# Optimization experiments

Measured on AMD Instinct MI355X. Metric: run time of the kernel, lower is better.

The kernel has to match this reference:

```python
import jax, jax.numpy as jnp
import numpy as np
from jax import lax

B, T, D_MODEL = 4, 2048, 2048
EXPAND, D_CONV = 2, 4
D_INNER = D_MODEL * EXPAND


def setup_inputs() -> dict:
    key = jax.random.key(0)
    ks = jax.random.split(key, 5)
    x = jax.random.normal(ks[0], (B, T, D_MODEL), dtype=jnp.float32)
    w_in = jax.random.normal(ks[1], (2 * D_INNER, D_MODEL), dtype=jnp.float32) * (D_MODEL ** -0.5)
    w_out = jax.random.normal(ks[2], (D_MODEL, D_INNER), dtype=jnp.float32) * (D_INNER ** -0.5)
    conv_w = jax.random.normal(ks[3], (D_INNER, 1, D_CONV), dtype=jnp.float32) * (D_CONV ** -0.5)
    conv_b = jax.random.normal(ks[4], (D_INNER,), dtype=jnp.float32) * 0.02
    D = jnp.ones((D_INNER,), dtype=jnp.float32)
    return {"x": x, "w_in": w_in, "w_out": w_out, "conv_w": conv_w, "conv_b": conv_b, "D": D}


def _forward(x, w_in, w_out, conv_w, conv_b, D):
    # in_proj: [B,T,C] @ [C, 2*d_inner]
    x_proj = jnp.einsum('btc,dc->btd', x, w_in)
    xi, gate = jnp.split(x_proj, 2, axis=-1)  # each [B,T,d_inner]
    # depthwise causal conv1d: torch pads both sides by d_conv-1 then truncates
    # output to first T positions -> equivalent to left-pad (d_conv-1), valid conv.
    xc = jnp.transpose(xi, (0, 2, 1))  # [B, d_inner, T]
    xc = lax.conv_general_dilated(
        xc, conv_w,
        window_strides=(1,),
        padding=[(D_CONV - 1, 0)],
        dimension_numbers=('NCH', 'OIH', 'NCH'),
        feature_group_count=D_INNER,
    ) + conv_b[None, :, None]
    xc = jnp.transpose(xc, (0, 2, 1))  # [B, T, d_inner]
    h = jax.nn.silu(xc) * D[None, None, :] * jax.nn.silu(gate)
    return jnp.einsum('btd,cd->btc', h, w_out)


def reference(x, w_in, w_out, conv_w, conv_b, D):
    return _forward(x, w_in, w_out, conv_w, conv_b, D)
```

## Files before the change

kernel.cpp:

```cpp
#include <hip/hip_runtime.h>
#include <hip/hip_bf16.h>
#include <stdint.h>
#include <string.h>


#define BT_TOTAL 8192
#define DM 2048
#define DI 4096

typedef __attribute__((ext_vector_type(8)))  short short8;
typedef __attribute__((ext_vector_type(16))) float f32x16;

__device__ __forceinline__ void async_ld16(const void* g, void* l) {
    __builtin_amdgcn_global_load_lds(
        (__attribute__((address_space(1))) void*)g,
        (__attribute__((address_space(3))) void*)l,
        16, 0, 0);
}

__device__ __forceinline__ float bf2f(ushort u) {
    union { uint i; float f; } v; v.i = ((uint)u) << 16; return v.f;
}

__device__ __forceinline__ ushort f2bf_bits(float f) {
    union { __hip_bfloat16 b; ushort u; } v;
    v.b = __float2bfloat16(f);
    return v.u;
}

#define RA0 0
#define RB0 16384
#define RA1 32768
#define RB1 49152

#define BAR()   asm volatile("s_barrier" ::: "memory")
#define LGKM0() asm volatile("s_waitcnt lgkmcnt(0)" ::: "memory")
#define VM6()   asm volatile("s_waitcnt vmcnt(6)" ::: "memory")
#define VM0()   asm volatile("s_waitcnt vmcnt(0)" ::: "memory")
#define PRIO1() __builtin_amdgcn_s_setprio(1)
#define PRIO0() __builtin_amdgcn_s_setprio(0)

template<bool OUT_BF16>
__global__ __launch_bounds__(512, 2) void gemm256_kernel(
    const ushort* __restrict__ A, const ushort* __restrict__ B,
    void* __restrict__ Cp, int M, int N, int K)
{
    __shared__ ushort lds[65536];

    const int tid  = threadIdx.x;
    const int lane = tid & 63;
    const int wave = tid >> 6;
    const int wm   = wave >> 2;
    const int wn   = wave & 3;
    const int l31  = lane & 31;
    const int half = lane >> 5;

    const int nbx = gridDim.x;
    const int nwg = nbx * gridDim.y;
    int orig = blockIdx.y * nbx + blockIdx.x;
    orig = (orig & 7) * (nwg >> 3) + (orig >> 3);
    const int bn = (orig % nbx) * 256;
    const int bm = (orig / nbx) * 256;

    const int rq = tid >> 3;
    const int jq = tid & 7;
    const int fq = (rq ^ (rq >> 3)) & 7;
    const int goffA = (bm + rq) * K + ((jq ^ fq) * 8);
    const int goffB = (bn + rq) * K + ((jq ^ fq) * 8);
    const int dst8  = tid * 8;

    const int flane = (l31 ^ (l31 >> 3)) & 7;
    const int cl8   = (half ^ flane) * 8;
    const int aBase = (wm * 128 + l31) * 64;
    const int bBase = (wn * 64  + l31) * 64;

    f32x16 acc[4][2];
#pragma unroll
    for (int m = 0; m < 4; ++m)
#pragma unroll
        for (int n = 0; n < 2; ++n)
#pragma unroll
            for (int r = 0; r < 16; ++r)
                acc[m][n][r] = 0.f;

    short8 aE[4], aO[4], b0[4], b1[4];

#define STA(P, QROW, REG) async_ld16((P) + (size_t)(QROW) * K + goffA, \
                                     &lds[(REG) + (QROW) * 64 + dst8])
#define STB(P, QROW, REG) async_ld16((P) + (size_t)(QROW) * K + goffB, \
                                     &lds[(REG) + (QROW) * 64 + dst8])

#define RDA(MH, REG) do { \
    _Pragma("unroll") \
    for (int ks = 0; ks < 4; ++ks) { \
        aE[ks] = *(const short8*)&lds[(REG) + aBase + (MH)*4096 + (cl8 ^ (ks<<4))]; \
        aO[ks] = *(const short8*)&lds[(REG) + aBase + (MH)*4096 + 2048 + (cl8 ^ (ks<<4) ^ 32)]; \
    } } while (0)

#define RDB(DSTV, NF, REG) do { \
    _Pragma("unroll") \
    for (int ks = 0; ks < 4; ++ks) { \
        DSTV[ks] = *(const short8*)&lds[(REG) + bBase + (NF)*2048 + (cl8 ^ (ks<<4) ^ ((NF)<<5))]; \
    } } while (0)

#define MMA(MH, NH, BF) do { \
    _Pragma("unroll") \
    for (int ks = 0; ks < 4; ++ks) { \
        acc[(MH)*2    ][(NH)] = __builtin_amdgcn_mfma_f32_32x32x16_bf16( \
            aE[ks], BF[ks], acc[(MH)*2    ][(NH)], 0, 0, 0); \
        acc[(MH)*2 + 1][(NH)] = __builtin_amdgcn_mfma_f32_32x32x16_bf16( \
            aO[ks], BF[ks], acc[(MH)*2 + 1][(NH)], 0, 0, 0); \
    } } while (0)

    {
        STA(A, 0, RA0);  STA(A, 128, RA0);
        STB(B, 0, RB0);  STB(B, 128, RB0);
        STA(A, 64, RA0); STA(A, 192, RA0);
        STB(B, 64, RB0); STB(B, 192, RB0);
        const ushort* Ap = A + 64;
        const ushort* Bp = B + 64;
        STA(Ap, 0, RA1);  STA(Ap, 128, RA1);
        STB(Bp, 0, RB1);  STB(Bp, 128, RB1);
        STA(Ap, 64, RA1); STA(Ap, 192, RA1);
        VM6(); BAR();
    }

    const int NITER = K >> 7;
    for (int i = 0; i < NITER; ++i) {
        const bool last = (i == NITER - 1);
        const int k1 = 128 * i + 64;
        const int k2 = 128 * i + 128;
        const int k3 = 128 * i + 192;

        RDA(0, RA0); RDB(b0, 0, RB0);
        STB(B + k1, 64, RB1); STB(B + k1, 192, RB1);
        BAR(); LGKM0();
        PRIO1(); MMA(0, 0, b0); PRIO0();
        BAR();

        RDB(b1, 1, RB0);
        if (!last) { STA(A + k2, 0, RA0); STA(A + k2, 128, RA0); }
        BAR(); LGKM0();
        PRIO1(); MMA(0, 1, b1); PRIO0();
        BAR();

        RDA(1, RA0);
        if (!last) { STB(B + k2, 0, RB0); STB(B + k2, 128, RB0); }
        BAR(); LGKM0();
        PRIO1(); MMA(1, 1, b1); PRIO0();
        BAR();

        if (!last) { STA(A + k2, 64, RA0); STA(A + k2, 192, RA0); }
        BAR();
        PRIO1(); MMA(1, 0, b0); PRIO0();
        if (last) { VM0(); } else { VM6(); }
        BAR();

        RDA(0, RA1); RDB(b0, 0, RB1);
        if (!last) { STB(B + k2, 64, RB0); STB(B + k2, 192, RB0); }
        BAR(); LGKM0();
        PRIO1(); MMA(0, 0, b0); PRIO0();
        BAR();

        RDB(b1, 1, RB1);
        if (!last) { STA(A + k3, 0, RA1); STA(A + k3, 128, RA1); }
        BAR(); LGKM0();
        PRIO1(); MMA(0, 1, b1); PRIO0();
        BAR();

        RDA(1, RA1);
        if (!last) { STB(B + k3, 0, RB1); STB(B + k3, 128, RB1); }
        BAR(); LGKM0();
        PRIO1(); MMA(1, 1, b1); PRIO0();
        BAR();

        if (!last) { STA(A + k3, 64, RA1); STA(A + k3, 192, RA1); }
        BAR();
        PRIO1(); MMA(1, 0, b0); PRIO0();
        if (!last) { VM6(); BAR(); }
    }

    const int col0 = bn + wn * 64 + l31;
    const int row0 = bm + wm * 128 + 4 * half;
    if (OUT_BF16) {
        __hip_bfloat16* C = (__hip_bfloat16*)Cp;
#pragma unroll
        for (int m = 0; m < 4; ++m)
#pragma unroll
            for (int n = 0; n < 2; ++n)
#pragma unroll
                for (int r = 0; r < 16; ++r) {
                    const int row = row0 + m * 32 + (r & 3) + 8 * (r >> 2);
                    C[(size_t)row * (size_t)N + col0 + n * 32] =
                        __float2bfloat16(acc[m][n][r]);
                }
    } else {
        float* C = (float*)Cp;
#pragma unroll
        for (int m = 0; m < 4; ++m)
#pragma unroll
            for (int n = 0; n < 2; ++n)
#pragma unroll
                for (int r = 0; r < 16; ++r) {
                    const int row = row0 + m * 32 + (r & 3) + 8 * (r >> 2);
                    C[(size_t)row * (size_t)N + col0 + n * 32] = acc[m][n][r];
                }
    }
}

__global__ __launch_bounds__(256) void conv_silu_kernel(
    const ushort* __restrict__ xp,
    const float* __restrict__ cw,
    const float* __restrict__ cb,
    const float* __restrict__ Dv,
    ushort* __restrict__ h)
{
    const int v  = blockIdx.x * 256 + threadIdx.x;
    const int d8 = (v & 511) * 8;
    const int bt = v >> 9;
    const int t  = bt & 2047;

    const uint4 gv = *(const uint4*)(xp + (size_t)bt * (2 * DI) + DI + d8);
    uint4 tap[4];
#pragma unroll
    for (int k = 0; k < 4; ++k) {
        const int tt = t - 3 + k;
        if (tt >= 0)
            tap[k] = *(const uint4*)(xp + (size_t)(bt - 3 + k) * (2 * DI) + d8);
        else
            tap[k] = (uint4){0u, 0u, 0u, 0u};
    }

    const float4* cwv = (const float4*)(cw + (size_t)d8 * 4);
    const float4  cb0 = *(const float4*)(cb + d8);
    const float4  cb1 = *(const float4*)(cb + d8 + 4);
    const float4  dv0 = *(const float4*)(Dv + d8);
    const float4  dv1 = *(const float4*)(Dv + d8 + 4);
    const float cbs[8] = {cb0.x, cb0.y, cb0.z, cb0.w, cb1.x, cb1.y, cb1.z, cb1.w};
    const float dvs[8] = {dv0.x, dv0.y, dv0.z, dv0.w, dv1.x, dv1.y, dv1.z, dv1.w};

    ushort res[8];
#pragma unroll
    for (int j = 0; j < 8; ++j) {
        float a = cbs[j];
        const float4 w = cwv[j];
        const float wk[4] = {w.x, w.y, w.z, w.w};
#pragma unroll
        for (int k = 0; k < 4; ++k) {
            const uint u = ((const uint*)&tap[k])[j >> 1];
            const ushort us = (j & 1) ? (ushort)(u >> 16) : (ushort)(u & 0xffff);
            a += bf2f(us) * wk[k];
        }
        const uint gu = ((const uint*)&gv)[j >> 1];
        const ushort gs = (j & 1) ? (ushort)(gu >> 16) : (ushort)(gu & 0xffff);
        const float g = bf2f(gs);
        const float sc = a / (1.f + __expf(-a));
        const float sg = g / (1.f + __expf(-g));
        res[j] = f2bf_bits(sc * dvs[j] * sg);
    }
    *(uint4*)(h + (size_t)bt * DI + d8) = *(const uint4*)res;
}

__global__ __launch_bounds__(256) void f32_to_bf16_x4(
    const float* __restrict__ in, __hip_bfloat16* __restrict__ out, int n4)
{
    const int i = blockIdx.x * 256 + threadIdx.x;
    if (i >= n4) return;
    const float4 v = *(const float4*)(in + (size_t)i * 4);
    union { __hip_bfloat16 hh[4]; ushort4 u; } cv;
    cv.hh[0] = __float2bfloat16(v.x);
    cv.hh[1] = __float2bfloat16(v.y);
    cv.hh[2] = __float2bfloat16(v.z);
    cv.hh[3] = __float2bfloat16(v.w);
    *(ushort4*)((ushort*)out + (size_t)i * 4) = cv.u;
}

extern "C" void kernel_launch(void* const* d_in, const int* in_sizes, int n_in,
                              void* d_out, int out_size, void* d_ws, size_t ws_size,
                              hipStream_t stream)
{
    const float* x     = (const float*)d_in[0];
    const float* w_in  = (const float*)d_in[1];
    const float* w_out = (const float*)d_in[2];
    const float* cw    = (const float*)d_in[3];
    const float* cb    = (const float*)d_in[4];
    const float* Dv    = (const float*)d_in[5];
    float* out = (float*)d_out;

    char* wsc = (char*)d_ws;
    __hip_bfloat16* xproj = (__hip_bfloat16*)wsc;
    __hip_bfloat16* xb    = (__hip_bfloat16*)(wsc + (size_t)134217728);
    __hip_bfloat16* winb  = (__hip_bfloat16*)(wsc + (size_t)134217728 + 33554432);
    __hip_bfloat16* hbuf  = (__hip_bfloat16*)(wsc + (size_t)134217728);
    __hip_bfloat16* woutb = (__hip_bfloat16*)(wsc + (size_t)201326592);

    f32_to_bf16_x4<<<(BT_TOTAL * DM / 4 + 255) / 256, 256, 0, stream>>>(x, xb, BT_TOTAL * DM / 4);
    f32_to_bf16_x4<<<(2 * DI * DM / 4 + 255) / 256, 256, 0, stream>>>(w_in, winb, 2 * DI * DM / 4);
    f32_to_bf16_x4<<<(DM * DI / 4 + 255) / 256, 256, 0, stream>>>(w_out, woutb, DM * DI / 4);

    gemm256_kernel<true><<<dim3((2 * DI) / 256, BT_TOTAL / 256), 512, 0, stream>>>(
        (const ushort*)xb, (const ushort*)winb, xproj, BT_TOTAL, 2 * DI, DM);

    conv_silu_kernel<<<(BT_TOTAL * DI / 8) / 256, 256, 0, stream>>>(
        (const ushort*)xproj, cw, cb, Dv, (ushort*)hbuf);

    gemm256_kernel<false><<<dim3(DM / 256, BT_TOTAL / 256), 512, 0, stream>>>(
        (const ushort*)hbuf, (const ushort*)woutb, out, BT_TOTAL, DM, DI);
}
```

Baseline: 646.5 us.

## Double-buffer A fragments in registers and drop per-phase barriers and lgkm waits

Adds separate register sets for both A halves and loads both B halves up front, so each LDS read phase overlaps the preceding MFMA phase. Removes the barrier plus explicit lgkmcnt(0) wait before each MMA block, leaving one barrier per phase and relying on compiler-inserted waits. This cuts synchronization stalls in the GEMM main loop but raises VGPR pressure, which could hurt occupancy at 2 blocks of 512 threads. Removing barriers also risks LDS overwrite races between async stores and reads in other waves.

```diff
diff --git a/kernel.cpp b/kernel.cpp
--- a/kernel.cpp
+++ b/kernel.cpp
@@ -34,7 +34,6 @@
 #define RB1 49152
 
 #define BAR()   asm volatile("s_barrier" ::: "memory")
-#define LGKM0() asm volatile("s_waitcnt lgkmcnt(0)" ::: "memory")
 #define VM6()   asm volatile("s_waitcnt vmcnt(6)" ::: "memory")
 #define VM0()   asm volatile("s_waitcnt vmcnt(0)" ::: "memory")
 #define PRIO1() __builtin_amdgcn_s_setprio(1)
@@ -83,18 +82,18 @@
             for (int r = 0; r < 16; ++r)
                 acc[m][n][r] = 0.f;
 
-    short8 aE[4], aO[4], b0[4], b1[4];
+    short8 a0E[4], a0O[4], a1E[4], a1O[4], b0[4], b1[4];
 
 #define STA(P, QROW, REG) async_ld16((P) + (size_t)(QROW) * K + goffA, \
                                      &lds[(REG) + (QROW) * 64 + dst8])
 #define STB(P, QROW, REG) async_ld16((P) + (size_t)(QROW) * K + goffB, \
                                      &lds[(REG) + (QROW) * 64 + dst8])
 
-#define RDA(MH, REG) do { \
+#define RDA(DE, DO, MH, REG) do { \
     _Pragma("unroll") \
     for (int ks = 0; ks < 4; ++ks) { \
-        aE[ks] = *(const short8*)&lds[(REG) + aBase + (MH)*4096 + (cl8 ^ (ks<<4))]; \
-        aO[ks] = *(const short8*)&lds[(REG) + aBase + (MH)*4096 + 2048 + (cl8 ^ (ks<<4) ^ 32)]; \
+        DE[ks] = *(const short8*)&lds[(REG) + aBase + (MH)*4096 + (cl8 ^ (ks<<4))]; \
+        DO[ks] = *(const short8*)&lds[(REG) + aBase + (MH)*4096 + 2048 + (cl8 ^ (ks<<4) ^ 32)]; \
     } } while (0)
 
 #define RDB(DSTV, NF, REG) do { \
@@ -103,13 +102,13 @@
         DSTV[ks] = *(const short8*)&lds[(REG) + bBase + (NF)*2048 + (cl8 ^ (ks<<4) ^ ((NF)<<5))]; \
     } } while (0)
 
-#define MMA(MH, NH, BF) do { \
+#define MMA(MH, NH, AE, AO, BF) do { \
     _Pragma("unroll") \
     for (int ks = 0; ks < 4; ++ks) { \
         acc[(MH)*2    ][(NH)] = __builtin_amdgcn_mfma_f32_32x32x16_bf16( \
-            aE[ks], BF[ks], acc[(MH)*2    ][(NH)], 0, 0, 0); \
+            AE[ks], BF[ks], acc[(MH)*2    ][(NH)], 0, 0, 0); \
         acc[(MH)*2 + 1][(NH)] = __builtin_amdgcn_mfma_f32_32x32x16_bf16( \
-            aO[ks], BF[ks], acc[(MH)*2 + 1][(NH)], 0, 0, 0); \
+            AO[ks], BF[ks], acc[(MH)*2 + 1][(NH)], 0, 0, 0); \
     } } while (0)
 
     {
@@ -132,51 +131,45 @@
         const int k2 = 128 * i + 128;
         const int k3 = 128 * i + 192;
 
-        RDA(0, RA0); RDB(b0, 0, RB0);
+        RDA(a0E, a0O, 0, RA0);
+        RDB(b0, 0, RB0);
+        RDB(b1, 1, RB0);
         STB(B + k1, 64, RB1); STB(B + k1, 192, RB1);
-        BAR(); LGKM0();
-        PRIO1(); MMA(0, 0, b0); PRIO0();
-        BAR();
-
-        RDB(b1, 1, RB0);
+        PRIO1(); MMA(0, 0, a0E, a0O, b0); PRIO0();
+        BAR();
+
+        RDA(a1E, a1O, 1, RA0);
         if (!last) { STA(A + k2, 0, RA0); STA(A + k2, 128, RA0); }
-        BAR(); LGKM0();
-        PRIO1(); MMA(0, 1, b1); PRIO0();
-        BAR();
-
-        RDA(1, RA0);
+        PRIO1(); MMA(0, 1, a0E, a0O, b1); PRIO0();
+        BAR();
+
         if (!last) { STB(B + k2, 0, RB0); STB(B + k2, 128, RB0); }
-        BAR(); LGKM0();
-        PRIO1(); MMA(1, 1, b1); PRIO0();
+        PRIO1(); MMA(1, 1, a1E, a1O, b1); PRIO0();
         BAR();
 
         if (!last) { STA(A + k2, 64, RA0); STA(A + k2, 192, RA0); }
-        BAR();
-        PRIO1(); MMA(1, 0, b0); PRIO0();
+        PRIO1(); MMA(1, 0, a1E, a1O, b0); PRIO0();
         if (last) { VM0(); } else { VM6(); }
         BAR();
 
-        RDA(0, RA1); RDB(b0, 0, RB1);
+        RDA(a0E, a0O, 0, RA1);
+        RDB(b0, 0, RB1);
+        RDB(b1, 1, RB1);
         if (!last) { STB(B + k2, 64, RB0); STB(B + k2, 192, RB0); }
-        BAR(); LGKM0();
-        PRIO1(); MMA(0, 0, b0); PRIO0();
-        BAR();
-
-        RDB(b1, 1, RB1);
+        PRIO1(); MMA(0, 0, a0E, a0O, b0); PRIO0();
+        BAR();
+
+        RDA(a1E, a1O, 1, RA1);
         if (!last) { STA(A + k3, 0, RA1); STA(A + k3, 128, RA1); }
-        BAR(); LGKM0();
-        PRIO1(); MMA(0, 1, b1); PRIO0();
-        BAR();
-
-        RDA(1, RA1);
+        PRIO1(); MMA(0, 1, a0E, a0O, b1); PRIO0();
+        BAR();
+
         if (!last) { STB(B + k3, 0, RB1); STB(B + k3, 128, RB1); }
-        BAR(); LGKM0();
-        PRIO1(); MMA(1, 1, b1); PRIO0();
+        PRIO1(); MMA(1, 1, a1E, a1O, b1); PRIO0();
         BAR();
 
         if (!last) { STA(A + k3, 64, RA1); STA(A + k3, 192, RA1); }
-        BAR();
-        PRIO1(); MMA(1, 0, b0); PRIO0();
+        PRIO1(); MMA(1, 0, a1E, a1O, b0); PRIO0();
         if (!last) { VM6(); BAR(); }
     }
 
```

Measured after the change: 993.1 us. 53.6% more time.
